# Kernel optimization log

Measured on AMD Instinct MI355X. Metric: run time of the kernel, lower is better.

Reference implementation:

```python
import jax, jax.numpy as jnp
import numpy as np
from jax import lax

HEADS, DIM_HEAD, LANDMARKS, PINV_ITERS = 8, 64, 256, 6
D = 512


def layernorm(x, w, b, eps=1e-5):
    mu = x.mean(-1, keepdims=True)
    var = ((x - mu) ** 2).mean(-1, keepdims=True)
    return (x - mu) * lax.rsqrt(var + eps) * w + b


def pinv_iter(x, iters=PINV_ITERS):
    # Moore-Penrose pseudo-inverse via Newton-Schulz (lucidrains nystrom-attention)
    abs_x = jnp.abs(x)
    z = jnp.swapaxes(x, -1, -2) / (jnp.max(abs_x.sum(-1)) * jnp.max(abs_x.sum(-2)))
    I = jnp.eye(x.shape[-1], dtype=x.dtype)
    for _ in range(iters):
        xz = x @ z
        z = 0.25 * z @ (13 * I - xz @ (15 * I - xz @ (7 * I - xz)))
    return z


def nystrom_attention(x, qkv_w, out_w, out_b, res_w):
    b, n, _ = x.shape
    m = LANDMARKS
    pad = (m - n % m) % m
    xp = jnp.pad(x, ((0, 0), (pad, 0), (0, 0)))  # left-pad seq to multiple of m
    n_p = n + pad
    q, k, v = jnp.split(xp @ qkv_w, 3, axis=-1)
    split = lambda t: t.reshape(b, n_p, HEADS, DIM_HEAD).transpose(0, 2, 1, 3)
    q, k, v = split(q), split(k), split(v)  # (b, h, n_p, d)
    q = q * DIM_HEAD ** -0.5
    l = n_p // m  # tokens per landmark
    q_l = q.reshape(b, HEADS, m, l, DIM_HEAD).mean(3)  # (b, h, m, d)
    k_l = k.reshape(b, HEADS, m, l, DIM_HEAD).mean(3)
    a1 = jax.nn.softmax(jnp.einsum('bhnd,bhmd->bhnm', q, k_l), -1)  # (b,h,n_p,m)
    a2 = jax.nn.softmax(jnp.einsum('bhmd,bhld->bhml', q_l, k_l), -1)  # (b,h,m,m)
    a3 = jax.nn.softmax(jnp.einsum('bhmd,bhnd->bhmn', q_l, k), -1)  # (b,h,m,n_p)
    out = (a1 @ pinv_iter(a2)) @ (a3 @ v)  # (b,h,n_p,d)
    # depthwise residual conv over the seq dim, kernel (33,1), one per head
    res = lax.conv_general_dilated(v, res_w, (1, 1), [(16, 16), (0, 0)],
                                   dimension_numbers=('NCHW', 'OIHW', 'NCHW'),
                                   feature_group_count=HEADS)
    out = out + res
    out = out.transpose(0, 2, 1, 3).reshape(b, n_p, HEADS * DIM_HEAD)
    return (out @ out_w + out_b)[:, -n:]


def ppeg(x, Hh, Ww, w7, b7, w5, b5, w3, b3):
    B, _, C = x.shape
    cls_tok, feat = x[:, :1], x[:, 1:]
    f = feat.transpose(0, 2, 1).reshape(B, C, Hh, Ww)
    def dwconv(w, bb, p):
        return lax.conv_general_dilated(f, w, (1, 1), [(p, p), (p, p)],
                                        dimension_numbers=('NCHW', 'OIHW', 'NCHW'),
                                        feature_group_count=C) + bb[None, :, None, None]
    y = f + dwconv(w7, b7, 3) + dwconv(w5, b5, 2) + dwconv(w3, b3, 1)
    y = y.reshape(B, C, Hh * Ww).transpose(0, 2, 1)
    return jnp.concatenate([cls_tok, y], axis=1)


def setup_inputs() -> dict:
    key = jax.random.key(0)
    ks = jax.random.split(key, 16)
    E, NC, H = 1024, 4, HEADS
    f32 = jnp.float32
    rn = lambda k, shp, s=0.02: (jax.random.normal(k, shp, f32) * s)
    return {
        'x': jax.random.normal(ks[0], (1, 40960, E), f32),
        'fc1_w': rn(ks[1], (E, D)), 'fc1_b': jnp.zeros((D,), f32),
        'cls_token': jax.random.normal(ks[2], (1, 1, D), f32),
        'l1_norm_w': jnp.ones((D,), f32), 'l1_norm_b': jnp.zeros((D,), f32),
        'l1_qkv_w': rn(ks[3], (D, 3 * D)),
        'l1_out_w': rn(ks[4], (D, D)), 'l1_out_b': jnp.zeros((D,), f32),
        'l1_res_w': rn(ks[5], (H, 1, 33, 1), 0.1),
        'ppeg_w7': rn(ks[6], (D, 1, 7, 7), 0.1), 'ppeg_b7': jnp.zeros((D,), f32),
        'ppeg_w5': rn(ks[7], (D, 1, 5, 5), 0.1), 'ppeg_b5': jnp.zeros((D,), f32),
        'ppeg_w3': rn(ks[8], (D, 1, 3, 3), 0.1), 'ppeg_b3': jnp.zeros((D,), f32),
        'l2_norm_w': jnp.ones((D,), f32), 'l2_norm_b': jnp.zeros((D,), f32),
        'l2_qkv_w': rn(ks[9], (D, 3 * D)),
        'l2_out_w': rn(ks[10], (D, D)), 'l2_out_b': jnp.zeros((D,), f32),
        'l2_res_w': rn(ks[11], (H, 1, 33, 1), 0.1),
        'norm_w': jnp.ones((D,), f32), 'norm_b': jnp.zeros((D,), f32),
        'fc3_w': rn(ks[12], (D, NC)), 'fc3_b': jnp.zeros((NC,), f32),
    }


def reference(x, fc1_w, fc1_b, cls_token, l1_norm_w, l1_norm_b, l1_qkv_w, l1_out_w, l1_out_b, l1_res_w, ppeg_w7, ppeg_b7, ppeg_w5, ppeg_b5, ppeg_w3, ppeg_b3, l2_norm_w, l2_norm_b, l2_qkv_w, l2_out_w, l2_out_b, l2_res_w, norm_w, norm_b, fc3_w, fc3_b):
    B, N, E = x.shape  # (1, 40960, 1024)
    POOL_OUT = 20480
    # AdaptiveMaxPool2d((20480, E)) on a (1, N, E) tensor: max-pool seq dim N -> 20480
    ft = x.reshape(B, POOL_OUT, N // POOL_OUT, E).max(axis=2)
    ft = jax.nn.relu(ft @ fc1_w + fc1_b)  # (1, 20480, 512)
    Hn = ft.shape[1]
    _H = int(np.ceil(np.sqrt(Hn)))  # 144
    add = _H * _H - Hn  # 256
    ft = jnp.concatenate([ft, ft[:, :add]], axis=1)  # (1, 20736, 512)
    h = jnp.concatenate([jnp.broadcast_to(cls_token, (B, 1, D)), ft], axis=1)  # 20737 tokens
    h = h + nystrom_attention(layernorm(h, l1_norm_w, l1_norm_b), l1_qkv_w, l1_out_w, l1_out_b, l1_res_w)
    h = ppeg(h, _H, _H, ppeg_w7, ppeg_b7, ppeg_w5, ppeg_b5, ppeg_w3, ppeg_b3)
    h = h + nystrom_attention(layernorm(h, l2_norm_w, l2_norm_b), l2_qkv_w, l2_out_w, l2_out_b, l2_res_w)
    h = layernorm(h, norm_w, norm_b)[:, 0]
    logits = h @ fc3_w + fc3_b
    return logits, jax.nn.softmax(logits, -1), jnp.argmax(logits, -1)
```

## Files before the change

kernel.cpp:

```cpp
#include <hip/hip_runtime.h>


constexpr int D_    = 512;
constexpr int E_    = 1024;
constexpr int NTOK  = 20737;
constexpr int NP_   = 20992;
constexpr int NH_   = 8;
constexpr int HD_   = 64;
constexpr int MLM   = 256;
constexpr int LCH   = 82;
constexpr int HHW   = 144;
constexpr int NFEAT = 20736;
constexpr int PADR  = 255;
constexpr int NCH   = 41;
constexpr int CHTOK = 512;

typedef __attribute__((ext_vector_type(8))) short bf16x8;
typedef __attribute__((ext_vector_type(4))) float f32x4;

__device__ __forceinline__ unsigned short f2bf(float f){
  unsigned int u = __float_as_uint(f);
  unsigned int r = u + 0x7fffu + ((u >> 16) & 1u);
  return (unsigned short)(r >> 16);
}
__device__ __forceinline__ float bfu(unsigned short u){
  return __uint_as_float((unsigned int)u << 16);
}

__device__ __forceinline__ float waveMaxF(float v){
#pragma unroll
  for (int o = 32; o > 0; o >>= 1) v = fmaxf(v, __shfl_xor(v, o));
  return v;
}
__device__ __forceinline__ float waveSumF(float v){
#pragma unroll
  for (int o = 32; o > 0; o >>= 1) v += __shfl_xor(v, o);
  return v;
}
__device__ __forceinline__ float blockMax256(float v, float* sbuf){
  v = waveMaxF(v);
  if ((threadIdx.x & 63) == 0) sbuf[threadIdx.x >> 6] = v;
  __syncthreads();
  float r = fmaxf(fmaxf(sbuf[0], sbuf[1]), fmaxf(sbuf[2], sbuf[3]));
  __syncthreads();
  return r;
}
__device__ __forceinline__ float blockSum256(float v, float* sbuf){
  v = waveSumF(v);
  if ((threadIdx.x & 63) == 0) sbuf[threadIdx.x >> 6] = v;
  __syncthreads();
  float r = sbuf[0] + sbuf[1] + sbuf[2] + sbuf[3];
  __syncthreads();
  return r;
}

__global__ __launch_bounds__(256) void wtrans_kernel(
    const float* __restrict__ W, unsigned short* __restrict__ Wt, int K, int N){
  __shared__ float tile[32][33];
  const int kb = blockIdx.x * 32, nb = blockIdx.y * 32;
  const int tx = threadIdx.x, ty = threadIdx.y;
  for (int i = ty; i < 32; i += 8) tile[i][tx] = W[(size_t)(kb + i) * N + nb + tx];
  __syncthreads();
  for (int i = ty; i < 32; i += 8)
    Wt[(size_t)(nb + i) * K + kb + tx] = f2bf(tile[tx][i]);
}

__global__ __launch_bounds__(256) void pool_bf16_kernel(
    const float* __restrict__ x, unsigned short* __restrict__ Ah){
  size_t idx4 = ((size_t)blockIdx.x * 256 + threadIdx.x) * 4;
  size_t m = idx4 >> 10, e = idx4 & 1023;
  float4 a = *(const float4*)(x + (m * 2) * E_ + e);
  float4 b = *(const float4*)(x + (m * 2 + 1) * E_ + e);
  unsigned long long pk =
      (unsigned long long)f2bf(fmaxf(a.x, b.x))
    | ((unsigned long long)f2bf(fmaxf(a.y, b.y)) << 16)
    | ((unsigned long long)f2bf(fmaxf(a.z, b.z)) << 32)
    | ((unsigned long long)f2bf(fmaxf(a.w, b.w)) << 48);
  *(unsigned long long*)(Ah + idx4) = pk;
}

__device__ __forceinline__ void mfma_tile128(
    const unsigned short* __restrict__ A, int arows, int bm,
    const unsigned short* __restrict__ Bt, int bn, int K,
    f32x4 acc[4][4], unsigned short* As, unsigned short* Bs){
  const int t = threadIdx.x;
  const int lane = t & 63, wave = t >> 6;
  const int wr = wave >> 1, wc = wave & 1;
  const int m16 = lane & 15, quad = lane >> 4;
  for (int kc = 0; kc < K; kc += 64){
    for (int idx = t; idx < 1024; idx += 256){
      int row = idx >> 3, off = (idx & 7) * 8;
      int ga = bm + row;
      ulonglong2 av = {0ull, 0ull};
      if (ga < arows) av = *(const ulonglong2*)(A + (size_t)ga * K + kc + off);
      *(ulonglong2*)(As + row * 72 + off) = av;
      ulonglong2 bv = *(const ulonglong2*)(Bt + (size_t)(bn + row) * K + kc + off);
      *(ulonglong2*)(Bs + row * 72 + off) = bv;
    }
    __syncthreads();
#pragma unroll
    for (int k2 = 0; k2 < 64; k2 += 32){
      bf16x8 af[4], bf[4];
#pragma unroll
      for (int mi = 0; mi < 4; mi++)
        af[mi] = *(const bf16x8*)(As + (wr * 64 + mi * 16 + m16) * 72 + k2 + quad * 8);
#pragma unroll
      for (int ni = 0; ni < 4; ni++)
        bf[ni] = *(const bf16x8*)(Bs + (wc * 64 + ni * 16 + m16) * 72 + k2 + quad * 8);
#pragma unroll
      for (int mi = 0; mi < 4; mi++)
#pragma unroll
        for (int ni = 0; ni < 4; ni++)
          acc[mi][ni] = __builtin_amdgcn_mfma_f32_16x16x32_bf16(af[mi], bf[ni], acc[mi][ni], 0, 0, 0);
    }
    __syncthreads();
  }
}

__global__ __launch_bounds__(256) void fc1_mfma_kernel(
    const unsigned short* __restrict__ Ah, const unsigned short* __restrict__ Bt,
    const float* __restrict__ bias, float* __restrict__ h){
  __shared__ unsigned short As[128 * 72], Bs[128 * 72];
  f32x4 z4 = {0.f, 0.f, 0.f, 0.f};
  f32x4 acc[4][4];
#pragma unroll
  for (int i = 0; i < 4; i++)
#pragma unroll
    for (int j = 0; j < 4; j++) acc[i][j] = z4;
  const int bm = blockIdx.x * 128, bn = blockIdx.y * 128;
  mfma_tile128(Ah, 20480, bm, Bt, bn, E_, acc, As, Bs);
  const int lane = threadIdx.x & 63, wave = threadIdx.x >> 6;
  const int wr = wave >> 1, wc = wave & 1;
  const int m16 = lane & 15, quad = lane >> 4;
#pragma unroll
  for (int mi = 0; mi < 4; mi++)
#pragma unroll
    for (int ni = 0; ni < 4; ni++){
      int col = bn + wc * 64 + ni * 16 + m16;
      float bv = bias[col];
#pragma unroll
      for (int r = 0; r < 4; r++){
        int row = bm + wr * 64 + mi * 16 + quad * 4 + r;
        float vv = fmaxf(acc[mi][ni][r] + bv, 0.f);
        h[(size_t)(1 + row) * D_ + col] = vv;
        if (row < 256) h[(size_t)(20481 + row) * D_ + col] = vv;
      }
    }
}

__global__ void cls_kernel(const float* __restrict__ cls, float* __restrict__ h){
  int c = blockIdx.x * 256 + threadIdx.x;
  if (c < D_) h[c] = cls[c];
}

__global__ void row0_copy_kernel(const float* __restrict__ src, float* __restrict__ dst){
  int c = blockIdx.x * 256 + threadIdx.x;
  if (c < D_) dst[c] = src[c];
}

__global__ __launch_bounds__(256) void ln_pad_kernel(
    const float* __restrict__ h, const float* __restrict__ w,
    const float* __restrict__ b, unsigned short* __restrict__ xph){
  const int wv = threadIdx.x >> 6, lane = threadIdx.x & 63;
  const int r = blockIdx.x * 4 + wv;
  unsigned int* xp32 = (unsigned int*)xph;
  if (r < PADR){
    uint4 z = {0u, 0u, 0u, 0u};
    *(uint4*)(xp32 + (size_t)r * 256 + lane * 4) = z;
    return;
  }
  const float* x = h + (size_t)(r - PADR) * D_;
  float4 a0 = *(const float4*)(x + lane * 8);
  float4 a1 = *(const float4*)(x + lane * 8 + 4);
  float s = (a0.x + a0.y) + (a0.z + a0.w) + (a1.x + a1.y) + (a1.z + a1.w);
  float mu = waveSumF(s) * (1.f / 512.f);
  float d[8] = {a0.x - mu, a0.y - mu, a0.z - mu, a0.w - mu,
                a1.x - mu, a1.y - mu, a1.z - mu, a1.w - mu};
  float vs = 0.f;
#pragma unroll
  for (int i = 0; i < 8; i++) vs += d[i] * d[i];
  float var = waveSumF(vs) * (1.f / 512.f);
  float rs = rsqrtf(var + 1e-5f);
  float4 w0 = *(const float4*)(w + lane * 8);
  float4 w1 = *(const float4*)(w + lane * 8 + 4);
  float4 b0 = *(const float4*)(b + lane * 8);
  float4 b1 = *(const float4*)(b + lane * 8 + 4);
  float wv8[8] = {w0.x, w0.y, w0.z, w0.w, w1.x, w1.y, w1.z, w1.w};
  float bv8[8] = {b0.x, b0.y, b0.z, b0.w, b1.x, b1.y, b1.z, b1.w};
  uint4 pk;
  unsigned int* pkp = (unsigned int*)&pk;
#pragma unroll
  for (int i = 0; i < 4; i++){
    unsigned int lo = f2bf(d[2 * i] * rs * wv8[2 * i] + bv8[2 * i]);
    unsigned int hi = f2bf(d[2 * i + 1] * rs * wv8[2 * i + 1] + bv8[2 * i + 1]);
    pkp[i] = lo | (hi << 16);
  }
  *(uint4*)(xp32 + (size_t)r * 256 + lane * 4) = pk;
}

__global__ __launch_bounds__(256) void qkv_mfma_kernel(
    const unsigned short* __restrict__ A, const unsigned short* __restrict__ Bt,
    unsigned short* __restrict__ q16, unsigned short* __restrict__ k16,
    unsigned short* __restrict__ v16){
  __shared__ unsigned short As[128 * 72], Bs[128 * 72];
  f32x4 z4 = {0.f, 0.f, 0.f, 0.f};
  f32x4 acc[4][4];
#pragma unroll
  for (int i = 0; i < 4; i++)
#pragma unroll
    for (int j = 0; j < 4; j++) acc[i][j] = z4;
  const int bm = blockIdx.x * 128, bn = blockIdx.y * 128;
  mfma_tile128(A, NP_, bm, Bt, bn, D_, acc, As, Bs);
  const int lane = threadIdx.x & 63, wave = threadIdx.x >> 6;
  const int wr = wave >> 1, wc = wave & 1;
  const int m16 = lane & 15, quad = lane >> 4;
#pragma unroll
  for (int mi = 0; mi < 4; mi++)
#pragma unroll
    for (int ni = 0; ni < 4; ni++){
      int col = bn + wc * 64 + ni * 16 + m16;
      int which = col >> 9, hh = (col >> 6) & 7, d = col & 63;
      size_t cbase = (size_t)hh * NP_ * HD_ + d;
      unsigned short* dst;
      float sc = 1.f;
      if (which == 0){ dst = q16; sc = 0.125f; }
      else if (which == 1) dst = k16;
      else dst = v16;
#pragma unroll
      for (int r = 0; r < 4; r++){
        int row = bm + wr * 64 + mi * 16 + quad * 4 + r;
        dst[cbase + (size_t)row * HD_] = f2bf(acc[mi][ni][r] * sc);
      }
    }
}

__global__ __launch_bounds__(256) void landmark_kernel(
    const unsigned short* __restrict__ q16, const unsigned short* __restrict__ k16,
    float* __restrict__ ql, float* __restrict__ kl,
    unsigned short* __restrict__ qlh, unsigned short* __restrict__ klh){
  const int wv = threadIdx.x >> 6, d = threadIdx.x & 63;
  const int im = blockIdx.x * 4 + wv, h = blockIdx.y;
  size_t base = ((size_t)h * NP_ + (size_t)im * LCH) * HD_ + d;
  float sq = 0.f, sk = 0.f;
  for (int r = 0; r < LCH; r++){
    sq += bfu(q16[base + (size_t)r * HD_]);
    sk += bfu(k16[base + (size_t)r * HD_]);
  }
  float qm = sq * (1.f / 82.f), km = sk * (1.f / 82.f);
  size_t oidx = ((size_t)h * MLM + im) * HD_ + d;
  ql[oidx] = qm;  qlh[oidx] = f2bf(qm);
  kl[oidx] = km;  klh[oidx] = f2bf(km);
}

__global__ __launch_bounds__(256) void a2_kernel(
    const float* __restrict__ ql, const float* __restrict__ kl,
    float* __restrict__ a2, unsigned short* __restrict__ a2h,
    unsigned short* __restrict__ a2l){
  const int im = blockIdx.x, h = blockIdx.y, t = threadIdx.x;
  __shared__ __align__(16) float qs[64];
  __shared__ float s4[4];
  if (t < 64) qs[t] = ql[((size_t)h * MLM + im) * HD_ + t];
  __syncthreads();
  const float4* kr4 = (const float4*)(kl + ((size_t)h * MLM + t) * HD_);
  const float4* qs4 = (const float4*)qs;
  float s = 0.f;
#pragma unroll
  for (int d4 = 0; d4 < 16; d4++){
    float4 kv = kr4[d4], qv = qs4[d4];
    s += qv.x*kv.x + qv.y*kv.y + qv.z*kv.z + qv.w*kv.w;
  }
  float mx = blockMax256(s, s4);
  float e = __expf(s - mx);
  float S = blockSum256(e, s4);
  float v = e / S;
  size_t idx = ((size_t)h * MLM + im) * MLM + t;
  a2[idx] = v;
  unsigned short hi = f2bf(v);
  a2h[idx] = hi;
  a2l[idx] = f2bf(v - bfu(hi));
}

__global__ __launch_bounds__(256) void pinv_scale_kernel(
    const float* __restrict__ a2, float* __restrict__ scal){
  const int h = blockIdx.x, j = threadIdx.x;
  const float* A = a2 + (size_t)h * MLM * MLM;
  float cs = 0.f;
  for (int t = 0; t < MLM; t++) cs += A[(size_t)t * MLM + j];
  __shared__ float s4[4];
  float cmax = blockMax256(cs, s4);
  if (j == 0) scal[h] = cmax;
}

__global__ __launch_bounds__(256) void pinv_init_kernel(
    const float* __restrict__ a2, const float* __restrict__ scal,
    unsigned short* __restrict__ zh, unsigned short* __restrict__ zl,
    unsigned short* __restrict__ zth, unsigned short* __restrict__ ztl){
  const int i = blockIdx.x, h = blockIdx.y, j = threadIdx.x;
  float cmax = scal[0];
#pragma unroll
  for (int hh = 1; hh < 8; hh++) cmax = fmaxf(cmax, scal[hh]);
  float inv = 1.f / cmax;
  size_t idx = ((size_t)h * MLM + i) * MLM + j;
  float vr = a2[((size_t)h * MLM + j) * MLM + i] * inv;
  float vt = a2[idx] * inv;
  unsigned short hi = f2bf(vr);
  zh[idx] = hi; zl[idx] = f2bf(vr - bfu(hi));
  hi = f2bf(vt);
  zth[idx] = hi; ztl[idx] = f2bf(vt - bfu(hi));
}

__global__ __launch_bounds__(256) void bmm256_split_kernel(
    const unsigned short* __restrict__ Ahg, const unsigned short* __restrict__ Alg,
    const unsigned short* __restrict__ Bthg, const unsigned short* __restrict__ Btlg,
    float c0, float c1,
    unsigned short* __restrict__ Crh, unsigned short* __restrict__ Crl,
    unsigned short* __restrict__ Cth, unsigned short* __restrict__ Ctl,
    float* __restrict__ Cf, unsigned int tsgn){
  __shared__ __align__(16) unsigned short Ash[32 * 72], Asl[32 * 72];
  __shared__ __align__(16) unsigned short Bsh[32 * 72], Bsl[32 * 72];
  const int bid = blockIdx.x;
  const int h = bid & 7;
  const int tid2 = bid >> 3;
  const int bm = (tid2 & 7) * 32;
  const int bn = (tid2 >> 3) * 32;
  const int t = threadIdx.x, lane = t & 63, w = t >> 6;
  const int wr = w >> 1, wc = w & 1, m16 = lane & 15, quad = lane >> 4;
  const size_t hb = (size_t)h * 65536;
  const unsigned short* gAh0 = Ahg + hb + (size_t)bm * 256;
  const unsigned short* gAl0 = Alg + hb + (size_t)bm * 256;
  const unsigned short* gBh0 = Bthg + hb + (size_t)bn * 256;
  const unsigned short* gBl0 = Btlg + hb + (size_t)bn * 256;
  const int srow = t >> 3, soff = (t & 7) * 8;
  const int sl = srow * 72 + soff;
  f32x4 acc = {0.f, 0.f, 0.f, 0.f};
  for (int kc = 0; kc < 256; kc += 64){
    {
      size_t g = (size_t)srow * 256 + kc + soff;
      *(uint4*)(Ash + sl) = *(const uint4*)(gAh0 + g);
      *(uint4*)(Asl + sl) = *(const uint4*)(gAl0 + g);
      *(uint4*)(Bsh + sl) = *(const uint4*)(gBh0 + g);
      *(uint4*)(Bsl + sl) = *(const uint4*)(gBl0 + g);
    }
    __syncthreads();
    if (c0 != 0.f && (bn & ~63) == kc){
      if (t < 32){
        int kloc = bn - kc + t;
        float v = c0 + bfu(Bsh[t * 72 + kloc]) + bfu(Bsl[t * 72 + kloc]);
        unsigned short hi = f2bf(v);
        Bsh[t * 72 + kloc] = hi;
        Bsl[t * 72 + kloc] = f2bf(v - bfu(hi));
      }
      __syncthreads();
    }
#pragma unroll
    for (int k2 = 0; k2 < 64; k2 += 32){
      bf16x8 ah = *(const bf16x8*)(Ash + (wr * 16 + m16) * 72 + k2 + quad * 8);
      bf16x8 al = *(const bf16x8*)(Asl + (wr * 16 + m16) * 72 + k2 + quad * 8);
      bf16x8 bh = *(const bf16x8*)(Bsh + (wc * 16 + m16) * 72 + k2 + quad * 8);
      bf16x8 bl = *(const bf16x8*)(Bsl + (wc * 16 + m16) * 72 + k2 + quad * 8);
      acc = __builtin_amdgcn_mfma_f32_16x16x32_bf16(ah, bh, acc, 0, 0, 0);
      acc = __builtin_amdgcn_mfma_f32_16x16x32_bf16(ah, bl, acc, 0, 0, 0);
      acc = __builtin_amdgcn_mfma_f32_16x16x32_bf16(al, bh, acc, 0, 0, 0);
    }
    __syncthreads();
  }
#pragma unroll
  for (int r = 0; r < 4; r++){
    int row = bm + wr * 16 + quad * 4 + r;
    int col = bn + wc * 16 + m16;
    float v = c1 * acc[r];
    unsigned short hi = f2bf(v);
    unsigned short lo = f2bf(v - bfu(hi));
    size_t rm = hb + (size_t)row * 256 + col;
    if (Crh){ Crh[rm] = hi; Crl[rm] = lo; }
    if (Cth){
      size_t tm = hb + (size_t)col * 256 + row;
      Cth[tm] = hi ^ (unsigned short)tsgn;
      Ctl[tm] = lo ^ (unsigned short)tsgn;
    }
    if (Cf) Cf[rm] = v;
  }
}

__global__ __launch_bounds__(256) void a3v_part_kernel(
    const unsigned short* __restrict__ qlh, const unsigned short* __restrict__ k16,
    const unsigned short* __restrict__ v16, float* __restrict__ pacc,
    float* __restrict__ pml){
  __shared__ __align__(16) unsigned short qs16[64 * 72];
  __shared__ __align__(16) unsigned short kb16[64 * 72];
  __shared__ __align__(16) unsigned short vt16[64 * 72];
  const int bid = blockIdx.x;
  const int h = bid & 7;
  const int j = bid >> 3;
  const int lt = j & 3;
  const int ch = j >> 2;
  const int t = threadIdx.x;
  const int lane = t & 63, w = t >> 6;
  const int m16 = lane & 15, quad = lane >> 4;

  const unsigned short* qg = qlh + ((size_t)h * MLM + lt * 64) * HD_;
  for (int idx = t; idx < 512; idx += 256){
    int row = idx >> 3, off = (idx & 7) * 8;
    *(uint4*)(qs16 + row * 72 + off) = *(const uint4*)(qg + (size_t)row * HD_ + off);
  }
  f32x4 z4 = {0.f, 0.f, 0.f, 0.f};
  f32x4 acc_o[4] = {z4, z4, z4, z4};
  float mreg[4], lreg[4];
#pragma unroll
  for (int r = 0; r < 4; r++){ mreg[r] = -3.0e38f; lreg[r] = 0.f; }
  const unsigned short* kg = k16 + ((size_t)h * NP_ + ch * CHTOK) * HD_;
  const unsigned short* vg = v16 + ((size_t)h * NP_ + ch * CHTOK) * HD_;

  for (int sc = 0; sc < 8; sc++){
    __syncthreads();
    for (int idx = t; idx < 512; idx += 256){
      int row = idx >> 3, off = (idx & 7) * 8;
      *(uint4*)(kb16 + row * 72 + off) =
          *(const uint4*)(kg + (size_t)(sc * 64 + row) * HD_ + off);
      uint4 pv = *(const uint4*)(vg + (size_t)(sc * 64 + row) * HD_ + off);
      unsigned int uu[4] = {pv.x, pv.y, pv.z, pv.w};
#pragma unroll
      for (int jj = 0; jj < 4; jj++){
        vt16[(off + 2 * jj)     * 72 + row] = (unsigned short)(uu[jj] & 0xffffu);
        vt16[(off + 2 * jj + 1) * 72 + row] = (unsigned short)(uu[jj] >> 16);
      }
    }
    __syncthreads();
    f32x4 acc_s[4] = {z4, z4, z4, z4};
#pragma unroll
    for (int kc = 0; kc < 64; kc += 32){
      bf16x8 a = *(const bf16x8*)(qs16 + (w * 16 + m16) * 72 + kc + quad * 8);
#pragma unroll
      for (int ni = 0; ni < 4; ni++){
        bf16x8 b = *(const bf16x8*)(kb16 + (ni * 16 + m16) * 72 + kc + quad * 8);
        acc_s[ni] = __builtin_amdgcn_mfma_f32_16x16x32_bf16(a, b, acc_s[ni], 0, 0, 0);
      }
    }
    __syncthreads();
#pragma unroll
    for (int r = 0; r < 4; r++){
      float cm = fmaxf(fmaxf(acc_s[0][r], acc_s[1][r]), fmaxf(acc_s[2][r], acc_s[3][r]));
#pragma unroll
      for (int o = 1; o < 16; o <<= 1) cm = fmaxf(cm, __shfl_xor(cm, o));
      if (__any(cm > mreg[r])){
        float mn = fmaxf(mreg[r], cm);
        float scl = __expf(mreg[r] - mn);
        lreg[r] *= scl;
        acc_o[0][r] *= scl; acc_o[1][r] *= scl;
        acc_o[2][r] *= scl; acc_o[3][r] *= scl;
        mreg[r] = mn;
      }
      float mcur = mreg[r];
      float p0 = __expf(acc_s[0][r] - mcur), p1 = __expf(acc_s[1][r] - mcur);
      float p2 = __expf(acc_s[2][r] - mcur), p3 = __expf(acc_s[3][r] - mcur);
      float ls = (p0 + p1) + (p2 + p3);
#pragma unroll
      for (int o = 1; o < 16; o <<= 1) ls += __shfl_xor(ls, o);
      lreg[r] += ls;
      int prow = (w * 16 + quad * 4 + r) * 72 + m16;
      kb16[prow + 0]  = f2bf(p0);
      kb16[prow + 16] = f2bf(p1);
      kb16[prow + 32] = f2bf(p2);
      kb16[prow + 48] = f2bf(p3);
    }
    __syncthreads();
#pragma unroll
    for (int kc = 0; kc < 64; kc += 32){
      bf16x8 a = *(const bf16x8*)(kb16 + (w * 16 + m16) * 72 + kc + quad * 8);
#pragma unroll
      for (int ni = 0; ni < 4; ni++){
        bf16x8 b = *(const bf16x8*)(vt16 + (ni * 16 + m16) * 72 + kc + quad * 8);
        acc_o[ni] = __builtin_amdgcn_mfma_f32_16x16x32_bf16(a, b, acc_o[ni], 0, 0, 0);
      }
    }
  }
#pragma unroll
  for (int r = 0; r < 4; r++){
    int im = lt * 64 + w * 16 + quad * 4 + r;
    size_t base = ((size_t)h * NCH + ch) * MLM + im;
#pragma unroll
    for (int ni = 0; ni < 4; ni++)
      pacc[base * HD_ + ni * 16 + m16] = acc_o[ni][r];
    if (m16 == 0){
      pml[base * 2]     = mreg[r];
      pml[base * 2 + 1] = lreg[r];
    }
  }
}

__global__ __launch_bounds__(64) void a3v_combine_kernel(
    const float* __restrict__ pacc, const float* __restrict__ pml,
    float* __restrict__ t1){
  const int im = blockIdx.x, h = blockIdx.y, lane = threadIdx.x;
  float M = -3.0e38f;
  for (int c = 0; c < NCH; c++)
    M = fmaxf(M, pml[(((size_t)h * NCH + c) * MLM + im) * 2]);
  float accv = 0.f, L = 0.f;
  for (int c = 0; c < NCH; c++){
    size_t base = ((size_t)h * NCH + c) * MLM + im;
    float mc = pml[base * 2], lc = pml[base * 2 + 1];
    float w = __expf(mc - M);
    accv += w * pacc[base * HD_ + lane];
    L += w * lc;
  }
  t1[((size_t)h * MLM + im) * HD_ + lane] = accv / L;
}

__global__ __launch_bounds__(256) void zt1_kernel(
    const float* __restrict__ z, const float* __restrict__ t1,
    unsigned short* __restrict__ t2t){
  const int h = blockIdx.y;
  const int t = threadIdx.x;
  const int d = t & 63, ri = t >> 6;
  const int im = blockIdx.x * 4 + ri;
  const float* zr = z + ((size_t)h * MLM + im) * MLM;
  const float* t1h = t1 + (size_t)h * MLM * HD_;
  float acc = 0.f;
#pragma unroll 8
  for (int kk = 0; kk < MLM; kk++) acc += zr[kk] * t1h[(size_t)kk * HD_ + d];
  t2t[((size_t)h * HD_ + d) * MLM + im] = f2bf(acc);
}

__global__ __launch_bounds__(256) void out_tile_kernel(
    const unsigned short* __restrict__ q16, const unsigned short* __restrict__ klh,
    const unsigned short* __restrict__ t2t, const unsigned short* __restrict__ v16,
    const float* __restrict__ resw, unsigned short* __restrict__ outh){
  __shared__ __align__(16) unsigned short smem[64 * 72 * 2 + 64 * 264];
  unsigned short* qs16 = smem;
  unsigned short* kb16 = smem + 64 * 72;
  unsigned short* Ps   = smem + 64 * 72 * 2;
  const int bid = blockIdx.x;
  const int h = bid & 7, tile = bid >> 3;
  const int n0 = PADR + tile * 64;
  const int t = threadIdx.x;
  const int lane = t & 63, w = t >> 6;
  const int m16 = lane & 15, quad = lane >> 4;

  {
    const unsigned short* qh = q16 + (size_t)h * NP_ * HD_;
    for (int idx = t; idx < 512; idx += 256){
      int row = idx >> 3, off = (idx & 7) * 8;
      int n = n0 + row;
      uint4 val = {0u, 0u, 0u, 0u};
      if (n < NP_) val = *(const uint4*)(qh + (size_t)n * HD_ + off);
      *(uint4*)(qs16 + row * 72 + off) = val;
    }
  }
  f32x4 z4 = {0.f, 0.f, 0.f, 0.f};
  f32x4 acc_s[16];
#pragma unroll
  for (int i = 0; i < 16; i++) acc_s[i] = z4;
  const unsigned short* klg = klh + (size_t)h * MLM * HD_;
  for (int m = 0; m < 4; m++){
    __syncthreads();
    for (int idx = t; idx < 512; idx += 256){
      int row = idx >> 3, off = (idx & 7) * 8;
      *(uint4*)(kb16 + row * 72 + off) =
          *(const uint4*)(klg + (size_t)(m * 64 + row) * HD_ + off);
    }
    __syncthreads();
#pragma unroll
    for (int kc = 0; kc < 64; kc += 32){
      bf16x8 a = *(const bf16x8*)(qs16 + (w * 16 + m16) * 72 + kc + quad * 8);
#pragma unroll
      for (int ni = 0; ni < 4; ni++){
        bf16x8 b = *(const bf16x8*)(kb16 + (ni * 16 + m16) * 72 + kc + quad * 8);
        acc_s[m * 4 + ni] = __builtin_amdgcn_mfma_f32_16x16x32_bf16(a, b, acc_s[m * 4 + ni], 0, 0, 0);
      }
    }
  }
  __syncthreads();
#pragma unroll
  for (int r = 0; r < 4; r++){
    float mx = acc_s[0][r];
#pragma unroll
    for (int mc = 1; mc < 16; mc++) mx = fmaxf(mx, acc_s[mc][r]);
#pragma unroll
    for (int o = 1; o < 16; o <<= 1) mx = fmaxf(mx, __shfl_xor(mx, o));
    float p[16]; float sum = 0.f;
#pragma unroll
    for (int mc = 0; mc < 16; mc++){ p[mc] = __expf(acc_s[mc][r] - mx); sum += p[mc]; }
#pragma unroll
    for (int o = 1; o < 16; o <<= 1) sum += __shfl_xor(sum, o);
    float inv = 1.f / sum;
    int prow = (w * 16 + quad * 4 + r) * 264;
#pragma unroll
    for (int mc = 0; mc < 16; mc++)
      Ps[prow + (mc >> 2) * 64 + (mc & 3) * 16 + m16] = f2bf(p[mc] * inv);
  }
  f32x4 acc_o[4] = {z4, z4, z4, z4};
  const unsigned short* t2g = t2t + (size_t)h * HD_ * MLM;
  for (int ch = 0; ch < 4; ch++){
    __syncthreads();
    {
      int row = t >> 2, c8 = (t & 3) * 16;
      const unsigned short* src = t2g + (size_t)row * MLM + ch * 64 + c8;
      *(uint4*)(kb16 + row * 72 + c8)     = *(const uint4*)src;
      *(uint4*)(kb16 + row * 72 + c8 + 8) = *(const uint4*)(src + 8);
    }
    __syncthreads();
#pragma unroll
    for (int kc = 0; kc < 64; kc += 32){
      bf16x8 a = *(const bf16x8*)(Ps + (w * 16 + m16) * 264 + ch * 64 + kc + quad * 8);
#pragma unroll
      for (int ni = 0; ni < 4; ni++){
        bf16x8 b = *(const bf16x8*)(kb16 + (ni * 16 + m16) * 72 + kc + quad * 8);
        acc_o[ni] = __builtin_amdgcn_mfma_f32_16x16x32_bf16(a, b, acc_o[ni], 0, 0, 0);
      }
    }
  }
  __syncthreads();
  float* Obuf = (float*)Ps;
  unsigned short* vtile = (unsigned short*)(Obuf + 64 * 66);
#pragma unroll
  for (int r = 0; r < 4; r++){
    int row = w * 16 + quad * 4 + r;
#pragma unroll
    for (int ni = 0; ni < 4; ni++)
      Obuf[row * 66 + ni * 16 + m16] = acc_o[ni][r];
  }
  {
    const unsigned short* vh = v16 + (size_t)h * NP_ * HD_;
    for (int idx = t; idx < 768; idx += 256){
      int row = idx >> 3, off = (idx & 7) * 8;
      int nn = n0 - 16 + row;
      uint4 val = {0u, 0u, 0u, 0u};
      if (nn < NP_) val = *(const uint4*)(vh + (size_t)nn * HD_ + off);
      *(uint4*)(vtile + row * 72 + off) = val;
    }
  }
  __syncthreads();
  float wreg[33];
  {
    const float* wr = resw + h * 33;
#pragma unroll
    for (int kk = 0; kk < 33; kk++) wreg[kk] = wr[kk];
  }
  const int ty = t >> 4, tx = t & 15;
#pragma unroll
  for (int i = 0; i < 4; i++){
    int lrow = ty * 4 + i;
    float c0v = 0.f, c1v = 0.f, c2v = 0.f, c3v = 0.f;
    for (int kk = 0; kk < 33; kk++){
      uint2 uv = *(const uint2*)(vtile + (lrow + kk) * 72 + tx * 4);
      float wv = wreg[kk];
      c0v += __uint_as_float(uv.x << 16) * wv;
      c1v += __uint_as_float(uv.x & 0xffff0000u) * wv;
      c2v += __uint_as_float(uv.y << 16) * wv;
      c3v += __uint_as_float(uv.y & 0xffff0000u) * wv;
    }
    int trow = tile * 64 + lrow;
    if (trow < NTOK){
      const float* orow = Obuf + lrow * 66 + tx * 4;
      unsigned long long pk =
          (unsigned long long)f2bf(orow[0] + c0v)
        | ((unsigned long long)f2bf(orow[1] + c1v) << 16)
        | ((unsigned long long)f2bf(orow[2] + c2v) << 32)
        | ((unsigned long long)f2bf(orow[3] + c3v) << 48);
      *(unsigned long long*)(outh + (size_t)trow * D_ + h * HD_ + tx * 4) = pk;
    }
  }
}

__global__ __launch_bounds__(256) void proj_mfma_kernel(
    const unsigned short* __restrict__ A, const unsigned short* __restrict__ Bt,
    const float* __restrict__ bias, float* __restrict__ h){
  __shared__ unsigned short As[128 * 72], Bs[128 * 72];
  f32x4 z4 = {0.f, 0.f, 0.f, 0.f};
  f32x4 acc[4][4];
#pragma unroll
  for (int i = 0; i < 4; i++)
#pragma unroll
    for (int j = 0; j < 4; j++) acc[i][j] = z4;
  const int bm = blockIdx.x * 128, bn = blockIdx.y * 128;
  mfma_tile128(A, NTOK, bm, Bt, bn, D_, acc, As, Bs);
  const int lane = threadIdx.x & 63, wave = threadIdx.x >> 6;
  const int wr = wave >> 1, wc = wave & 1;
  const int m16 = lane & 15, quad = lane >> 4;
#pragma unroll
  for (int mi = 0; mi < 4; mi++)
#pragma unroll
    for (int ni = 0; ni < 4; ni++){
      int col = bn + wc * 64 + ni * 16 + m16;
      float bv = bias[col];
#pragma unroll
      for (int r = 0; r < 4; r++){
        int row = bm + wr * 64 + mi * 16 + quad * 4 + r;
        if (row < NTOK) h[(size_t)row * D_ + col] += acc[mi][ni][r] + bv;
      }
    }
}

__global__ __launch_bounds__(512) void ppeg_combine_kernel(
    const float* __restrict__ w7, const float* __restrict__ b7,
    const float* __restrict__ w5, const float* __restrict__ b5,
    const float* __restrict__ w3, const float* __restrict__ b3,
    float* __restrict__ wcomb, float* __restrict__ bcomb){
  const int c = threadIdx.x;
#pragma unroll
  for (int i = 0; i < 7; i++){
#pragma unroll
    for (int j = 0; j < 7; j++){
      int di = i - 3, dj = j - 3;
      float wv = w7[(size_t)c * 49 + i * 7 + j];
      if (di >= -2 && di <= 2 && dj >= -2 && dj <= 2)
        wv += w5[(size_t)c * 25 + (di + 2) * 5 + (dj + 2)];
      if (di >= -1 && di <= 1 && dj >= -1 && dj <= 1)
        wv += w3[(size_t)c * 9 + (di + 1) * 3 + (dj + 1)];
      if (di == 0 && dj == 0) wv += 1.f;
      wcomb[(size_t)(i * 7 + j) * 512 + c] = wv;
    }
  }
  bcomb[c] = b7[c] + b5[c] + b3[c];
}

__global__ __launch_bounds__(512) void ppeg_conv_kernel(
    const float* __restrict__ h, const float* __restrict__ wcomb,
    const float* __restrict__ bcomb, float* __restrict__ h2){
  const int c = threadIdx.x;
  const int bid = blockIdx.x;
  const int xcd = bid & 7;
  const int idx = bid >> 3;
  const int y = xcd * 18 + idx / 18;
  const int x0 = (idx % 18) * 8;
  float wc[49];
#pragma unroll
  for (int kk = 0; kk < 49; kk++) wc[kk] = wcomb[(size_t)kk * 512 + c];
  float acc[8];
  const float bv = bcomb[c];
#pragma unroll
  for (int p = 0; p < 8; p++) acc[p] = bv;
#pragma unroll
  for (int i = 0; i < 7; i++){
    const int yy = y + i - 3;
    if (yy < 0 || yy >= HHW) continue;
    const float* hrow = h + (size_t)(1 + yy * HHW) * D_ + c;
    float line[14];
#pragma unroll
    for (int j = 0; j < 14; j++){
      const int xx = x0 + j - 3;
      line[j] = (xx >= 0 && xx < HHW) ? hrow[(size_t)xx * D_] : 0.f;
    }
#pragma unroll
    for (int p = 0; p < 8; p++)
#pragma unroll
      for (int j = 0; j < 7; j++)
        acc[p] += line[p + j] * wc[i * 7 + j];
  }
#pragma unroll
  for (int p = 0; p < 8; p++)
    h2[(size_t)(1 + y * HHW + x0 + p) * D_ + c] = acc[p];
}

__global__ __launch_bounds__(512) void final_kernel(
    const float* __restrict__ h, const float* __restrict__ w,
    const float* __restrict__ b, const float* __restrict__ fc3w,
    const float* __restrict__ fc3b, float* __restrict__ out){
  __shared__ float vec[512];
  __shared__ float s8[8];
  __shared__ float lg[4];
  const int t = threadIdx.x;
  float x = h[t];
  float v = waveSumF(x);
  if ((t & 63) == 0) s8[t >> 6] = v;
  __syncthreads();
  float sum = 0.f;
#pragma unroll
  for (int i = 0; i < 8; i++) sum += s8[i];
  float mu = sum * (1.f / 512.f);
  __syncthreads();
  float d = x - mu;
  v = waveSumF(d * d);
  if ((t & 63) == 0) s8[t >> 6] = v;
  __syncthreads();
  float var = 0.f;
#pragma unroll
  for (int i = 0; i < 8; i++) var += s8[i];
  var *= (1.f / 512.f);
  float rs = rsqrtf(var + 1e-5f);
  vec[t] = d * rs * w[t] + b[t];
  __syncthreads();
  if (t < 4){
    float acc = fc3b[t];
    for (int kk = 0; kk < 512; kk++) acc += vec[kk] * fc3w[kk * 4 + t];
    lg[t] = acc;
  }
  __syncthreads();
  if (t == 0){
    float m = fmaxf(fmaxf(lg[0], lg[1]), fmaxf(lg[2], lg[3]));
    float e[4], se = 0.f;
#pragma unroll
    for (int i = 0; i < 4; i++){ e[i] = __expf(lg[i] - m); se += e[i]; }
    int am = 0; float bm = lg[0];
#pragma unroll
    for (int i = 1; i < 4; i++) if (lg[i] > bm){ bm = lg[i]; am = i; }
#pragma unroll
    for (int i = 0; i < 4; i++){ out[i] = lg[i]; out[4 + i] = e[i] / se; }
    out[8] = (float)am;
  }
}

extern "C" void kernel_launch(void* const* d_in, const int* in_sizes, int n_in,
                              void* d_out, int out_size, void* d_ws, size_t ws_size,
                              hipStream_t stream) {
  const float* x       = (const float*)d_in[0];
  const float* fc1_w   = (const float*)d_in[1];
  const float* fc1_b   = (const float*)d_in[2];
  const float* cls_tok = (const float*)d_in[3];
  const float* l1_nw   = (const float*)d_in[4];
  const float* l1_nb   = (const float*)d_in[5];
  const float* l1_qkvw = (const float*)d_in[6];
  const float* l1_outw = (const float*)d_in[7];
  const float* l1_outb = (const float*)d_in[8];
  const float* l1_resw = (const float*)d_in[9];
  const float* ppeg_w7 = (const float*)d_in[10];
  const float* ppeg_b7 = (const float*)d_in[11];
  const float* ppeg_w5 = (const float*)d_in[12];
  const float* ppeg_b5 = (const float*)d_in[13];
  const float* ppeg_w3 = (const float*)d_in[14];
  const float* ppeg_b3 = (const float*)d_in[15];
  const float* l2_nw   = (const float*)d_in[16];
  const float* l2_nb   = (const float*)d_in[17];
  const float* l2_qkvw = (const float*)d_in[18];
  const float* l2_outw = (const float*)d_in[19];
  const float* l2_outb = (const float*)d_in[20];
  const float* l2_resw = (const float*)d_in[21];
  const float* norm_w  = (const float*)d_in[22];
  const float* norm_b  = (const float*)d_in[23];
  const float* fc3_w   = (const float*)d_in[24];
  const float* fc3_b   = (const float*)d_in[25];

  float* W = (float*)d_ws;
  size_t o = 0;
  float* hbuf = W + o; o += (size_t)NTOK * D_;
  float* xp   = W + o; o += (size_t)NP_ * D_;
  float* qb   = W + o; o += (size_t)NH_ * NP_ * HD_;
  float* kb   = W + o; o += (size_t)NH_ * NP_ * HD_;
  float* vb   = W + o; o += (size_t)NH_ * NP_ * HD_;
  float* qlb  = W + o; o += (size_t)NH_ * MLM * HD_;
  float* klb  = W + o; o += (size_t)NH_ * MLM * HD_;
  float* a2b  = W + o; o += (size_t)NH_ * MLM * MLM;
  float* zfin = W + o; o += (size_t)NH_ * MLM * MLM;
  float* t1b  = W + o; o += (size_t)NH_ * MLM * HD_;
  float* t2r  = W + o; o += (size_t)NH_ * MLM * HD_;
  float* scalf = W + o; o += 16;
  float* wcomb = W + o; o += 49 * 512;
  float* bcomb = W + o; o += 512;
  unsigned short* fc1_wt  = (unsigned short*)(W + o); o += (size_t)D_ * E_ / 2;
  unsigned short* qkv_wt1 = (unsigned short*)(W + o); o += (size_t)1536 * D_ / 2;
  unsigned short* qkv_wt2 = (unsigned short*)(W + o); o += (size_t)1536 * D_ / 2;
  unsigned short* out_wt1 = (unsigned short*)(W + o); o += (size_t)D_ * D_ / 2;
  unsigned short* out_wt2 = (unsigned short*)(W + o); o += (size_t)D_ * D_ / 2;
  unsigned short* qlh = (unsigned short*)(W + o); o += (size_t)NH_ * MLM * HD_ / 2;
  unsigned short* klh = (unsigned short*)(W + o); o += (size_t)NH_ * MLM * HD_ / 2;
  const size_t HM = (size_t)NH_ * MLM * MLM;
  unsigned short* usp = (unsigned short*)(W + o); o += 18 * HM / 2;
  unsigned short* a2sh  = usp; usp += HM;
  unsigned short* a2sl  = usp; usp += HM;
  unsigned short* tah_s = usp; usp += HM;
  unsigned short* tal_s = usp; usp += HM;
  unsigned short* tath_s = usp; usp += HM;
  unsigned short* tatl_s = usp; usp += HM;
  unsigned short* tbth_s = usp; usp += HM;
  unsigned short* tbtl_s = usp; usp += HM;
  unsigned short* tcth_s = usp; usp += HM;
  unsigned short* tctl_s = usp; usp += HM;
  unsigned short* zsh[2], *zsl[2], *zsth[2], *zstl[2];
  for (int s = 0; s < 2; s++){
    zsh[s]  = usp; usp += HM;
    zsl[s]  = usp; usp += HM;
    zsth[s] = usp; usp += HM;
    zstl[s] = usp; usp += HM;
  }
  float* hbuf2 = W + o; o += (size_t)NTOK * D_;

  unsigned short* xph = (unsigned short*)xp;
  float* pacc = xp;
  float* pml  = xp + (size_t)NH_ * NCH * MLM * HD_;
  unsigned short* outh = (unsigned short*)xp;
  unsigned short* Ah  = (unsigned short*)qb;
  unsigned short* q16 = (unsigned short*)qb;
  unsigned short* k16 = (unsigned short*)kb;
  unsigned short* v16 = (unsigned short*)vb;
  unsigned short* t2t = (unsigned short*)t2r;

  wtrans_kernel<<<dim3(E_ / 32, D_ / 32), dim3(32, 8), 0, stream>>>(fc1_w, fc1_wt, E_, D_);
  wtrans_kernel<<<dim3(D_ / 32, 1536 / 32), dim3(32, 8), 0, stream>>>(l1_qkvw, qkv_wt1, D_, 1536);
  wtrans_kernel<<<dim3(D_ / 32, 1536 / 32), dim3(32, 8), 0, stream>>>(l2_qkvw, qkv_wt2, D_, 1536);
  wtrans_kernel<<<dim3(D_ / 32, D_ / 32), dim3(32, 8), 0, stream>>>(l1_outw, out_wt1, D_, D_);
  wtrans_kernel<<<dim3(D_ / 32, D_ / 32), dim3(32, 8), 0, stream>>>(l2_outw, out_wt2, D_, D_);
  ppeg_combine_kernel<<<1, 512, 0, stream>>>(ppeg_w7, ppeg_b7, ppeg_w5, ppeg_b5,
                                             ppeg_w3, ppeg_b3, wcomb, bcomb);

  pool_bf16_kernel<<<20480, 256, 0, stream>>>(x, Ah);
  fc1_mfma_kernel<<<dim3(160, 4), 256, 0, stream>>>(Ah, fc1_wt, fc1_b, hbuf);
  cls_kernel<<<2, 256, 0, stream>>>(cls_tok, hbuf);

  auto run_layer = [&](float* hcur, const float* nw, const float* nb,
                       const unsigned short* qkvwt, const unsigned short* outwt,
                       const float* outb, const float* resw){
    ln_pad_kernel<<<NP_ / 4, 256, 0, stream>>>(hcur, nw, nb, xph);
    qkv_mfma_kernel<<<dim3(164, 12), 256, 0, stream>>>(xph, qkvwt, q16, k16, v16);
    landmark_kernel<<<dim3(64, 8), 256, 0, stream>>>(q16, k16, qlb, klb, qlh, klh);
    a2_kernel<<<dim3(256, 8), 256, 0, stream>>>(qlb, klb, a2b, a2sh, a2sl);
    pinv_scale_kernel<<<8, 256, 0, stream>>>(a2b, scalf);
    pinv_init_kernel<<<dim3(256, 8), 256, 0, stream>>>(a2b, scalf,
        zsh[0], zsl[0], zsth[0], zstl[0]);
    int c = 0;
    for (int it = 0; it < 6; it++){
      bmm256_split_kernel<<<512, 256, 0, stream>>>(
          a2sh, a2sl, zsth[c], zstl[c], 0.f, 1.f,
          tah_s, tal_s, tath_s, tatl_s, nullptr, 0x8000u);
      bmm256_split_kernel<<<512, 256, 0, stream>>>(
          tah_s, tal_s, tath_s, tatl_s, 7.f, 1.f,
          nullptr, nullptr, tbth_s, tbtl_s, nullptr, 0x8000u);
      bmm256_split_kernel<<<512, 256, 0, stream>>>(
          tah_s, tal_s, tbth_s, tbtl_s, 15.f, 1.f,
          nullptr, nullptr, tcth_s, tctl_s, nullptr, 0x8000u);
      bmm256_split_kernel<<<512, 256, 0, stream>>>(
          zsh[c], zsl[c], tcth_s, tctl_s, 13.f, 0.25f,
          zsh[c ^ 1], zsl[c ^ 1], zsth[c ^ 1], zstl[c ^ 1],
          (it == 5) ? zfin : nullptr, 0u);
      c ^= 1;
    }
    a3v_part_kernel<<<NCH * 32, 256, 0, stream>>>(qlh, k16, v16, pacc, pml);
    a3v_combine_kernel<<<dim3(256, 8), 64, 0, stream>>>(pacc, pml, t1b);
    zt1_kernel<<<dim3(64, 8), 256, 0, stream>>>(zfin, t1b, t2t);
    out_tile_kernel<<<325 * 8, 256, 0, stream>>>(q16, klh, t2t, v16, resw, outh);
    proj_mfma_kernel<<<dim3(163, 4), 256, 0, stream>>>(outh, outwt, outb, hcur);
  };

  run_layer(hbuf, l1_nw, l1_nb, qkv_wt1, out_wt1, l1_outb, l1_resw);
  ppeg_conv_kernel<<<2592, 512, 0, stream>>>(hbuf, wcomb, bcomb, hbuf2);
  row0_copy_kernel<<<2, 256, 0, stream>>>(hbuf, hbuf2);
  run_layer(hbuf2, l2_nw, l2_nb, qkv_wt2, out_wt2, l2_outb, l2_resw);
  final_kernel<<<1, 512, 0, stream>>>(hbuf2, norm_w, norm_b, fc3_w, fc3_b, (float*)d_out);
}
```

Measured before the change: 1.420 ms.

## Stage QKV epilogue through LDS and shrink pinv bmm tiles to one wave

The QKV GEMM epilogue now writes its bf16 results into shared memory first, then stores each row's 64-element head slice to global memory with 16-byte vector stores instead of scattered 2-byte stores. The 256x256 split-bf16 pinv matmul drops from 32x32 tiles with four waves to 16x16 tiles with a single wave, launching four times as many blocks to spread the small per-iteration matmuls over more CUs. pinv_init now reads a2 coalesced and writes the transposed copy, instead of reading it transposed. The changes add an extra LDS round trip and barrier in the QKV kernel, and the bmm tiles reload more A/B data per output element.

```diff
diff --git a/kernel.cpp b/kernel.cpp
--- a/kernel.cpp
+++ b/kernel.cpp
@@ -202,7 +202,9 @@
     const unsigned short* __restrict__ A, const unsigned short* __restrict__ Bt,
     unsigned short* __restrict__ q16, unsigned short* __restrict__ k16,
     unsigned short* __restrict__ v16){
-  __shared__ unsigned short As[128 * 72], Bs[128 * 72];
+  __shared__ __align__(16) unsigned short SM[128 * 72 * 2];
+  unsigned short* As = SM;
+  unsigned short* Bs = SM + 128 * 72;
   f32x4 z4 = {0.f, 0.f, 0.f, 0.f};
   f32x4 acc[4][4];
 #pragma unroll
@@ -211,27 +213,35 @@
     for (int j = 0; j < 4; j++) acc[i][j] = z4;
   const int bm = blockIdx.x * 128, bn = blockIdx.y * 128;
   mfma_tile128(A, NP_, bm, Bt, bn, D_, acc, As, Bs);
-  const int lane = threadIdx.x & 63, wave = threadIdx.x >> 6;
+  const int t = threadIdx.x;
+  const int lane = t & 63, wave = t >> 6;
   const int wr = wave >> 1, wc = wave & 1;
   const int m16 = lane & 15, quad = lane >> 4;
+  unsigned short* T = SM;
 #pragma unroll
   for (int mi = 0; mi < 4; mi++)
 #pragma unroll
     for (int ni = 0; ni < 4; ni++){
-      int col = bn + wc * 64 + ni * 16 + m16;
-      int which = col >> 9, hh = (col >> 6) & 7, d = col & 63;
-      size_t cbase = (size_t)hh * NP_ * HD_ + d;
-      unsigned short* dst;
-      float sc = 1.f;
-      if (which == 0){ dst = q16; sc = 0.125f; }
-      else if (which == 1) dst = k16;
-      else dst = v16;
+      int lc = wc * 64 + ni * 16 + m16;
+      float sc = ((bn + lc) >> 9) == 0 ? 0.125f : 1.f;
 #pragma unroll
       for (int r = 0; r < 4; r++){
-        int row = bm + wr * 64 + mi * 16 + quad * 4 + r;
-        dst[cbase + (size_t)row * HD_] = f2bf(acc[mi][ni][r] * sc);
+        int lrow = wr * 64 + mi * 16 + quad * 4 + r;
+        T[lrow * 136 + lc] = f2bf(acc[mi][ni][r] * sc);
       }
     }
+  __syncthreads();
+  {
+    int row = t >> 1, half = t & 1;
+    int col0 = bn + half * 64;
+    int which = col0 >> 9, hh = (col0 >> 6) & 7;
+    unsigned short* dst = which == 0 ? q16 : (which == 1 ? k16 : v16);
+    size_t gb = (size_t)hh * NP_ * HD_ + (size_t)(bm + row) * HD_;
+    const unsigned short* src = T + row * 136 + half * 64;
+#pragma unroll
+    for (int i = 0; i < 8; i++)
+      *(uint4*)(dst + gb + i * 8) = *(const uint4*)(src + i * 8);
+  }
 }
 
 __global__ __launch_bounds__(256) void landmark_kernel(
@@ -301,63 +311,67 @@
   for (int hh = 1; hh < 8; hh++) cmax = fmaxf(cmax, scal[hh]);
   float inv = 1.f / cmax;
   size_t idx = ((size_t)h * MLM + i) * MLM + j;
-  float vr = a2[((size_t)h * MLM + j) * MLM + i] * inv;
-  float vt = a2[idx] * inv;
-  unsigned short hi = f2bf(vr);
-  zh[idx] = hi; zl[idx] = f2bf(vr - bfu(hi));
-  hi = f2bf(vt);
-  zth[idx] = hi; ztl[idx] = f2bf(vt - bfu(hi));
-}
-
-__global__ __launch_bounds__(256) void bmm256_split_kernel(
+  float a = a2[idx] * inv;
+  unsigned short hi = f2bf(a);
+  unsigned short lo = f2bf(a - bfu(hi));
+  zth[idx] = hi; ztl[idx] = lo;
+  size_t tdx = ((size_t)h * MLM + j) * MLM + i;
+  zh[tdx] = hi; zl[tdx] = lo;
+}
+
+__global__ __launch_bounds__(64) void bmm256_split_kernel(
     const unsigned short* __restrict__ Ahg, const unsigned short* __restrict__ Alg,
     const unsigned short* __restrict__ Bthg, const unsigned short* __restrict__ Btlg,
     float c0, float c1,
     unsigned short* __restrict__ Crh, unsigned short* __restrict__ Crl,
     unsigned short* __restrict__ Cth, unsigned short* __restrict__ Ctl,
     float* __restrict__ Cf, unsigned int tsgn){
-  __shared__ __align__(16) unsigned short Ash[32 * 72], Asl[32 * 72];
-  __shared__ __align__(16) unsigned short Bsh[32 * 72], Bsl[32 * 72];
+  __shared__ __align__(16) unsigned short Ash[16 * 72], Asl[16 * 72];
+  __shared__ __align__(16) unsigned short Bsh[16 * 72], Bsl[16 * 72];
   const int bid = blockIdx.x;
   const int h = bid & 7;
-  const int tid2 = bid >> 3;
-  const int bm = (tid2 & 7) * 32;
-  const int bn = (tid2 >> 3) * 32;
-  const int t = threadIdx.x, lane = t & 63, w = t >> 6;
-  const int wr = w >> 1, wc = w & 1, m16 = lane & 15, quad = lane >> 4;
+  const int idx = bid >> 3;
+  const int bm = (idx & 15) * 16;
+  const int bn = (idx >> 4) * 16;
+  const int l = threadIdx.x;
+  const int m16 = l & 15, quad = l >> 4;
   const size_t hb = (size_t)h * 65536;
   const unsigned short* gAh0 = Ahg + hb + (size_t)bm * 256;
   const unsigned short* gAl0 = Alg + hb + (size_t)bm * 256;
   const unsigned short* gBh0 = Bthg + hb + (size_t)bn * 256;
   const unsigned short* gBl0 = Btlg + hb + (size_t)bn * 256;
-  const int srow = t >> 3, soff = (t & 7) * 8;
-  const int sl = srow * 72 + soff;
+  const int srow = l >> 2, sk = (l & 3) * 16;
   f32x4 acc = {0.f, 0.f, 0.f, 0.f};
   for (int kc = 0; kc < 256; kc += 64){
     {
-      size_t g = (size_t)srow * 256 + kc + soff;
-      *(uint4*)(Ash + sl) = *(const uint4*)(gAh0 + g);
-      *(uint4*)(Asl + sl) = *(const uint4*)(gAl0 + g);
-      *(uint4*)(Bsh + sl) = *(const uint4*)(gBh0 + g);
-      *(uint4*)(Bsl + sl) = *(const uint4*)(gBl0 + g);
+      size_t g = (size_t)srow * 256 + kc + sk;
+      int sl = srow * 72 + sk;
+      *(uint4*)(Ash + sl)     = *(const uint4*)(gAh0 + g);
+      *(uint4*)(Ash + sl + 8) = *(const uint4*)(gAh0 + g + 8);
+      *(uint4*)(Asl + sl)     = *(const uint4*)(gAl0 + g);
+      *(uint4*)(Asl + sl + 8) = *(const uint4*)(gAl0 + g + 8);
+      *(uint4*)(Bsh + sl)     = *(const uint4*)(gBh0 + g);
+      *(uint4*)(Bsh + sl + 8) = *(const uint4*)(gBh0 + g + 8);
+      *(uint4*)(Bsl + sl)     = *(const uint4*)(gBl0 + g);
+      *(uint4*)(Bsl + sl + 8) = *(const uint4*)(gBl0 + g + 8);
     }
     __syncthreads();
     if (c0 != 0.f && (bn & ~63) == kc){
-      if (t < 32){
-        int kloc = bn - kc + t;
-        float v = c0 + bfu(Bsh[t * 72 + kloc]) + bfu(Bsl[t * 72 + kloc]);
+      if (l < 16){
+        int kloc = (bn & 63) + l;
+        float v = c0 + bfu(Bsh[l * 72 + kloc]) + bfu(Bsl[l * 72 + kloc]);
         unsigned short hi = f2bf(v);
-        Bsh[t * 72 + kloc] = hi;
-        Bsl[t * 72 + kloc] = f2bf(v - bfu(hi));
+        Bsh[l * 72 + kloc] = hi;
+        Bsl[l * 72 + kloc] = f2bf(v - bfu(hi));
       }
       __syncthreads();
     }
 #pragma unroll
     for (int k2 = 0; k2 < 64; k2 += 32){
-      bf16x8 ah = *(const bf16x8*)(Ash + (wr * 16 + m16) * 72 + k2 + quad * 8);
-      bf16x8 al = *(const bf16x8*)(Asl + (wr * 16 + m16) * 72 + k2 + quad * 8);
-      bf16x8 bh = *(const bf16x8*)(Bsh + (wc * 16 + m16) * 72 + k2 + quad * 8);
-      bf16x8 bl = *(const bf16x8*)(Bsl + (wc * 16 + m16) * 72 + k2 + quad * 8);
+      bf16x8 ah = *(const bf16x8*)(Ash + m16 * 72 + k2 + quad * 8);
+      bf16x8 al = *(const bf16x8*)(Asl + m16 * 72 + k2 + quad * 8);
+      bf16x8 bh = *(const bf16x8*)(Bsh + m16 * 72 + k2 + quad * 8);
+      bf16x8 bl = *(const bf16x8*)(Bsl + m16 * 72 + k2 + quad * 8);
       acc = __builtin_amdgcn_mfma_f32_16x16x32_bf16(ah, bh, acc, 0, 0, 0);
       acc = __builtin_amdgcn_mfma_f32_16x16x32_bf16(ah, bl, acc, 0, 0, 0);
       acc = __builtin_amdgcn_mfma_f32_16x16x32_bf16(al, bh, acc, 0, 0, 0);
@@ -366,8 +380,8 @@
   }
 #pragma unroll
   for (int r = 0; r < 4; r++){
-    int row = bm + wr * 16 + quad * 4 + r;
-    int col = bn + wc * 16 + m16;
+    int row = bm + quad * 4 + r;
+    int col = bn + m16;
     float v = c1 * acc[r];
     unsigned short hi = f2bf(v);
     unsigned short lo = f2bf(v - bfu(hi));
@@ -908,16 +922,16 @@
         zsh[0], zsl[0], zsth[0], zstl[0]);
     int c = 0;
     for (int it = 0; it < 6; it++){
-      bmm256_split_kernel<<<512, 256, 0, stream>>>(
+      bmm256_split_kernel<<<2048, 64, 0, stream>>>(
           a2sh, a2sl, zsth[c], zstl[c], 0.f, 1.f,
           tah_s, tal_s, tath_s, tatl_s, nullptr, 0x8000u);
-      bmm256_split_kernel<<<512, 256, 0, stream>>>(
+      bmm256_split_kernel<<<2048, 64, 0, stream>>>(
           tah_s, tal_s, tath_s, tatl_s, 7.f, 1.f,
           nullptr, nullptr, tbth_s, tbtl_s, nullptr, 0x8000u);
-      bmm256_split_kernel<<<512, 256, 0, stream>>>(
+      bmm256_split_kernel<<<2048, 64, 0, stream>>>(
           tah_s, tal_s, tbth_s, tbtl_s, 15.f, 1.f,
           nullptr, nullptr, tcth_s, tctl_s, nullptr, 0x8000u);
-      bmm256_split_kernel<<<512, 256, 0, stream>>>(
+      bmm256_split_kernel<<<2048, 64, 0, stream>>>(
           zsh[c], zsl[c], tcth_s, tctl_s, 13.f, 0.25f,
           zsh[c ^ 1], zsl[c ^ 1], zsth[c ^ 1], zstl[c ^ 1],
           (it == 5) ? zfin : nullptr, 0u);
```

Result: slower. 1.452 ms (+2.3%).
